# Optimization experiments

Hardware: AMD Instinct MI355X
Metric: run time of the kernel (lower is better)

Reference implementation:

```python
import jax, jax.numpy as jnp
import numpy as np

D = 2048
N = 4096
HEAD = 2
DH = D // HEAD


def setup_inputs() -> dict:
    key = jax.random.key(0)
    ks = jax.random.split(key, 7)
    s = 0.02  # realistic init scale for weights
    x = jax.random.normal(ks[0], (1, N, D), jnp.float32)
    Wq1 = jax.random.normal(ks[1], (DH, DH), jnp.float32) * s
    Wq2 = jax.random.normal(ks[2], (DH, DH), jnp.float32) * s
    Wk1 = jax.random.normal(ks[3], (DH, DH), jnp.float32) * s
    Wk2 = jax.random.normal(ks[4], (DH, DH), jnp.float32) * s
    Wv1 = jax.random.normal(ks[5], (DH, DH), jnp.float32) * s
    Wv2 = jax.random.normal(ks[6], (DH, DH), jnp.float32) * s
    return {"x": x, "Wq1": Wq1, "Wq2": Wq2, "Wk1": Wk1, "Wk2": Wk2,
            "Wv1": Wv1, "Wv2": Wv2}


def _head(xh, Wq, Wk, Wv):
    # xh: [1, N, Dh]; Linear applies in @ W^T (no bias)
    q = (xh @ Wq.T)[0]                      # [N, Dh]
    k = (xh @ Wk.T)[0]                      # [N, Dh] (k reshaped to 2D in torch)
    v = (xh @ Wv.T)[0]                      # [N, Dh]
    # QK_T linear with weight dynamically set to k (detached in torch):
    Sc = q @ jax.lax.stop_gradient(k).T     # [N, N]
    # Sc_V linear on v^T with weight set to Sc (detached in torch):
    Sc = jax.lax.stop_gradient(Sc)
    return v.T @ Sc.T                       # [Dh, N]  == (Sc @ v)^T


def reference(x, Wq1, Wq2, Wk1, Wk2, Wv1, Wv2):
    Dh = Wq1.shape[0]
    x1, x2 = x[..., :Dh], x[..., Dh:]       # torch.chunk(x, 2, dim=2)
    o1 = _head(x1, Wq1, Wk1, Wv1)           # [Dh, N]
    o2 = _head(x2, Wq2, Wk2, Wv2)           # [Dh, N]
    out = jnp.concatenate([o1, o2], axis=0).T  # transpose(-2,-1).squeeze -> [N, D]
    return out
```

## Files before the change

### kernel.cpp

```cpp
#include <hip/hip_runtime.h>
#include <hip/hip_bf16.h>


using bf16 = __hip_bfloat16;
typedef __attribute__((ext_vector_type(8))) __bf16 bf16x8;
typedef __attribute__((ext_vector_type(8))) unsigned short u16x8;
typedef __attribute__((ext_vector_type(4))) float f32x4;

#define M1 (1024 * 1024)

struct GB {
    const bf16* A[8];
    const bf16* B[8];
    void*       C[8];
    int lda[8];
    int ldb[8];
};

__device__ __forceinline__ void gload_lds16(const void* g, void* l) {
    __builtin_amdgcn_global_load_lds(
        (const __attribute__((address_space(1))) void*)g,
        (__attribute__((address_space(3))) void*)l, 16, 0, 0);
}

template<int N>
__device__ __forceinline__ void waitv() {
    if constexpr (N == 4)      asm volatile("s_waitcnt vmcnt(4)" ::: "memory");
    else if constexpr (N == 3) asm volatile("s_waitcnt vmcnt(3)" ::: "memory");
    else                       asm volatile("s_waitcnt vmcnt(0)" ::: "memory");
}

template<int BM_, int BN_, typename OUT_T>
__device__ __forceinline__ void gemm_core(
    const bf16* __restrict__ A, int lda,
    const bf16* __restrict__ B, int ldb,
    OUT_T* __restrict__ C, int ldc,
    int m0, int n0, int Ksub,
    unsigned short* smem, int tid)
{
    auto As = (unsigned short(*)[BM_ * 32])smem;
    auto Bs = (unsigned short(*)[BN_ * 32])(smem + 2 * BM_ * 32);

    constexpr int MI = BM_ / 32;
    constexpr int NI = BN_ / 32;
    constexpr int NLOADS = (BM_ + BN_) / 64;

    const int lane = tid & 63;
    const int wave = tid >> 6;
    const int wm   = wave >> 1;
    const int wn   = wave & 1;
    const int fr = lane & 15;
    const int kg = lane >> 4;
    const int srow = tid >> 2;
    const int scol = (tid & 3) * 8;

    auto stage = [&](int buf, int kt) {
        #pragma unroll
        for (int r = 0; r < BM_ / 64; ++r)
            gload_lds16(A + (size_t)(m0 + r * 64 + srow) * lda + (kt + scol),
                        &As[buf][(r * 64 + srow) * 32 + scol]);
        #pragma unroll
        for (int r = 0; r < BN_ / 64; ++r)
            gload_lds16(B + (size_t)(n0 + r * 64 + srow) * ldb + (kt + scol),
                        &Bs[buf][(r * 64 + srow) * 32 + scol]);
    };

    f32x4 acc[MI][NI];
    #pragma unroll
    for (int i = 0; i < MI; ++i)
        #pragma unroll
        for (int j = 0; j < NI; ++j)
            acc[i][j] = {0.f, 0.f, 0.f, 0.f};

    const int niter = Ksub >> 5;
    int cur = 0;
    stage(0, 0);

    for (int it = 0; it < niter; ++it) {
        if (it + 1 < niter) {
            stage(cur ^ 1, (it + 1) << 5);
            waitv<NLOADS>();
        } else {
            waitv<0>();
        }
        __builtin_amdgcn_s_barrier();
        __builtin_amdgcn_sched_barrier(0);

        bf16x8 afrag[MI], bfrag[NI];
        #pragma unroll
        for (int mi = 0; mi < MI; ++mi)
            afrag[mi] = *(const bf16x8*)&As[cur][(wm * (BM_ / 2) + mi * 16 + fr) * 32 + kg * 8];
        #pragma unroll
        for (int ni = 0; ni < NI; ++ni)
            bfrag[ni] = *(const bf16x8*)&Bs[cur][(wn * (BN_ / 2) + ni * 16 + fr) * 32 + kg * 8];

        #pragma unroll
        for (int mi = 0; mi < MI; ++mi)
            #pragma unroll
            for (int ni = 0; ni < NI; ++ni)
                acc[mi][ni] = __builtin_amdgcn_mfma_f32_16x16x32_bf16(
                    afrag[mi], bfrag[ni], acc[mi][ni], 0, 0, 0);

        __builtin_amdgcn_sched_barrier(0);
        __builtin_amdgcn_s_barrier();
        __builtin_amdgcn_sched_barrier(0);
        cur ^= 1;
    }

    if constexpr (sizeof(OUT_T) == 2) {
        #pragma unroll
        for (int mi = 0; mi < MI; ++mi)
            #pragma unroll
            for (int ni = 0; ni < NI; ++ni) {
                const int c = wn * (BN_ / 2) + ni * 16 + fr;
                #pragma unroll
                for (int j = 0; j < 4; ++j) {
                    const int r = wm * (BM_ / 2) + mi * 16 + kg * 4 + j;
                    bf16 h = __float2bfloat16(acc[mi][ni][j]);
                    smem[r * BN_ + c] = *(unsigned short*)&h;
                }
            }
        __syncthreads();
        constexpr int V = (BM_ * BN_) / 2048;
        #pragma unroll
        for (int v = 0; v < V; ++v) {
            const int off = v * 2048 + tid * 8;
            const int r = off / BN_;
            const int c = off % BN_;
            *(u16x8*)((unsigned short*)C + (size_t)(m0 + r) * ldc + n0 + c) =
                *(const u16x8*)&smem[off];
        }
    } else {
        float* fs = (float*)smem;
        #pragma unroll
        for (int mi = 0; mi < MI; ++mi)
            #pragma unroll
            for (int ni = 0; ni < NI; ++ni) {
                const int c = wn * (BN_ / 2) + ni * 16 + fr;
                #pragma unroll
                for (int j = 0; j < 4; ++j) {
                    const int r = wm * (BM_ / 2) + mi * 16 + kg * 4 + j;
                    fs[r * BN_ + c] = acc[mi][ni][j];
                }
            }
        __syncthreads();
        constexpr int V = (BM_ * BN_) / 1024;
        #pragma unroll
        for (int v = 0; v < V; ++v) {
            const int off = v * 1024 + tid * 4;
            const int r = off / BN_;
            const int c = off % BN_;
            *(float4*)((float*)C + (size_t)(m0 + r) * ldc + n0 + c) =
                *(const float4*)&fs[off];
        }
    }
}

template<int BM_, int BN_, typename OUT_T>
__global__ __launch_bounds__(256, 4)
void gemm_bt_pa(GB g, int Ksub, int ldc)
{
    constexpr int STAGE_SH = 2 * (BM_ + BN_) * 32;
    constexpr int EPI_SH   = BM_ * BN_ * (int)sizeof(OUT_T) / 2;
    constexpr int SMEM_SH  = STAGE_SH > EPI_SH ? STAGE_SH : EPI_SH;
    __shared__ __align__(16) unsigned short smem[SMEM_SH];

    const int gx = gridDim.x, gy = gridDim.y;
    const int nwg = gx * gy * gridDim.z;
    const int orig = blockIdx.x + gx * (blockIdx.y + gy * blockIdx.z);
    const int cpx = nwg >> 3;
    const int wg = (orig & 7) * cpx + (orig >> 3);
    const int bx = wg % gx;
    const int by = (wg / gx) % gy;
    const int bz = wg / (gx * gy);

    gemm_core<BM_, BN_, OUT_T>(g.A[bz], g.lda[bz], g.B[bz], g.ldb[bz],
                               (OUT_T*)g.C[bz], ldc,
                               by * BM_, bx * BN_, Ksub,
                               smem, threadIdx.x);
}

struct B1Args {
    const bf16* xt;
    const bf16* wdst;
    bf16* Gp;
    bf16* Mp;
};

__global__ __launch_bounds__(256, 4)
void b1_kernel(B1Args a)
{
    __shared__ __align__(16) unsigned short smem[16384];

    const int nwg = 832;
    const int orig = blockIdx.x + 52 * blockIdx.z;
    const int cpx = nwg >> 3;
    const int wg = (orig & 7) * cpx + (orig >> 3);
    const int bx = wg % 52;
    const int bz = wg / 52;

    if (bx < 36) {
        const int h = bz >> 3, s = bz & 7;
        int ti = 0, rem = bx;
        while (rem >= 8 - ti) { rem -= 8 - ti; ++ti; }
        const int tj = ti + rem;
        const bf16* A = a.xt + (size_t)(h * 1024 + ti * 128) * 4096 + s * 512;
        const bf16* B = a.xt + (size_t)(h * 1024 + tj * 128) * 4096 + s * 512;
        bf16* C = a.Gp + ((size_t)bz * 36 + bx) * 16384;
        gemm_core<128, 128, bf16>(A, 4096, B, 4096, C, 128, 0, 0, 512,
                                  smem, threadIdx.x);
    } else {
        const int combo = bz & 3;
        const int h = combo >> 1, s = combo & 1;
        const int tile = (bz >> 2) * 16 + (bx - 36);
        const int m0 = (tile >> 3) * 128;
        const int n0 = (tile & 7) * 128;
        const bf16* A = a.wdst + (size_t)h * M1 + s * 512;
        const bf16* B = a.wdst + (size_t)(2 + h) * M1 + s * 512;
        bf16* C = a.Mp + (size_t)combo * M1;
        gemm_core<128, 128, bf16>(A, 1024, B, 1024, C, 1024, m0, n0, 512,
                                  smem, threadIdx.x);
    }
}


__device__ __forceinline__ ushort4 cvt4(float4 v) {
    ushort4 o; bf16 h;
    h = __float2bfloat16(v.x); o.x = *(unsigned short*)&h;
    h = __float2bfloat16(v.y); o.y = *(unsigned short*)&h;
    h = __float2bfloat16(v.z); o.z = *(unsigned short*)&h;
    h = __float2bfloat16(v.w); o.w = *(unsigned short*)&h;
    return o;
}

struct PrepArgs {
    const float* x;
    const float* w[4];
    const float* wv[2];
    bf16* xb;
    bf16* xt;
    bf16* wdst;
};

__device__ void xpose64(const float* __restrict__ src, int ldsrc,
                        int r0, int c0,
                        bf16* __restrict__ dstS, int ldS,
                        bf16* __restrict__ dstT, int ldT,
                        float (*tile)[65], int t)
{
    const int tr  = t >> 4;
    const int tc4 = (t & 15) * 4;
    #pragma unroll
    for (int ph = 0; ph < 4; ++ph) {
        const int row = ph * 16 + tr;
        float4 v = *(const float4*)(src + (size_t)(r0 + row) * ldsrc + c0 + tc4);
        tile[row][tc4 + 0] = v.x;
        tile[row][tc4 + 1] = v.y;
        tile[row][tc4 + 2] = v.z;
        tile[row][tc4 + 3] = v.w;
        if (dstS)
            *(ushort4*)((unsigned short*)dstS + (size_t)(r0 + row) * ldS + c0 + tc4) = cvt4(v);
    }
    __syncthreads();
    #pragma unroll
    for (int ph = 0; ph < 4; ++ph) {
        const int crow = ph * 16 + tr;
        float4 v = {tile[tc4 + 0][crow], tile[tc4 + 1][crow],
                    tile[tc4 + 2][crow], tile[tc4 + 3][crow]};
        *(ushort4*)((unsigned short*)dstT + (size_t)(c0 + crow) * ldT + r0 + tc4) = cvt4(v);
    }
}

__global__ void prep(PrepArgs p)
{
    __shared__ float tile[64][65];
    const int b = blockIdx.x;
    const int t = threadIdx.x;

    if (b < 2048) {
        const int n0 = (b & 63) * 64;
        const int c0 = (b >> 6) * 64;
        xpose64(p.x, 2048, n0, c0, p.xb, 2048, p.xt, 4096, tile, t);
    } else if (b < 3072) {
        const int i = b - 2048;
        const int mat = i >> 8;
        const int tl  = i & 255;
        const int r0 = (tl & 15) * 64;
        const int c0 = (tl >> 4) * 64;
        xpose64(p.w[mat], 1024, r0, c0, nullptr, 0,
                p.wdst + (size_t)mat * M1, 1024, tile, t);
    } else {
        const int i = b - 3072;
        const int mat = i >> 9;
        const int blk = i & 511;
        const size_t off = (size_t)blk * 2048 + t * 8;
        float4 v0 = *(const float4*)(p.wv[mat] + off);
        float4 v1 = *(const float4*)(p.wv[mat] + off + 4);
        unsigned short* d = (unsigned short*)p.wdst + (size_t)(4 + mat) * M1 + off;
        *(ushort4*)d       = cvt4(v0);
        *(ushort4*)(d + 4) = cvt4(v1);
    }
}


__device__ __forceinline__ void reduce_slices(const unsigned short* src,
                                              unsigned short* dst,
                                              int h, int r, int nslice)
{
    float acc[8] = {0, 0, 0, 0, 0, 0, 0, 0};
    for (int s = 0; s < nslice; ++s) {
        u16x8 v = *(const u16x8*)(src + ((size_t)(h * nslice + s) << 20) + r);
        #pragma unroll
        for (int j = 0; j < 8; ++j)
            acc[j] += __uint_as_float(((unsigned)v[j]) << 16);
    }
    u16x8 o;
    #pragma unroll
    for (int j = 0; j < 8; ++j) {
        bf16 hh = __float2bfloat16(acc[j]);
        o[j] = *(unsigned short*)&hh;
    }
    *(u16x8*)(dst + ((size_t)h << 20) + r) = o;
}

__global__ void reduce_GM(const unsigned short* Gp, const unsigned short* Mp,
                          unsigned short* Gd, unsigned short* Md)
{
    const int b = blockIdx.x, t = threadIdx.x;
    if (b < 576) {
        const int h    = b / 288;
        const int rem  = b - h * 288;
        const int tile = rem >> 3;
        const int blk  = rem & 7;
        int ti = 0, trem = tile;
        while (trem >= 8 - ti) { trem -= 8 - ti; ++ti; }
        const int tj = ti + trem;

        const int e  = blk * 2048 + t * 8;
        const int r  = e >> 7;
        const int c0 = e & 127;

        float acc[8] = {0, 0, 0, 0, 0, 0, 0, 0};
        for (int s = 0; s < 8; ++s) {
            u16x8 v = *(const u16x8*)(Gp + ((size_t)(h * 8 + s) * 36 + tile) * 16384 + e);
            #pragma unroll
            for (int j = 0; j < 8; ++j)
                acc[j] += __uint_as_float(((unsigned)v[j]) << 16);
        }
        u16x8 o;
        #pragma unroll
        for (int j = 0; j < 8; ++j) {
            bf16 hh = __float2bfloat16(acc[j]);
            o[j] = *(unsigned short*)&hh;
        }
        unsigned short* G = Gd + (size_t)h * M1;
        *(u16x8*)(G + (size_t)(ti * 128 + r) * 1024 + tj * 128 + c0) = o;
        if (ti != tj) {
            #pragma unroll
            for (int j = 0; j < 8; ++j)
                G[(size_t)(tj * 128 + c0 + j) * 1024 + ti * 128 + r] = o[j];
        }
    } else {
        const int e = ((b - 576) * 256 + t) * 8;
        reduce_slices(Mp, Md, e >> 20, e & (M1 - 1), 2);
    }
}

__global__ void reduce_4(const unsigned short* Sp, unsigned short* Dd)
{
    const int e = (blockIdx.x * 256 + threadIdx.x) * 8;
    reduce_slices(Sp, Dd, e >> 20, e & (M1 - 1), 4);
}


extern "C" void kernel_launch(void* const* d_in, const int* in_sizes, int n_in,
                              void* d_out, int out_size, void* d_ws, size_t ws_size,
                              hipStream_t stream)
{
    bf16* xb   = (bf16*)d_ws;
    bf16* xt   = xb + 8 * M1;
    bf16* wdst = xt + 8 * M1;
    bf16* Mp   = wdst + 6 * M1;
    bf16* Mb   = Mp + 4 * M1;
    bf16* Gb   = Mb + 2 * M1;
    bf16* Ytb  = Gb + 2 * M1;
    bf16* Utb  = Ytb + 2 * M1;

    bf16* scr = (bf16*)d_out;

    PrepArgs pa;
    pa.x = (const float*)d_in[0];
    pa.w[0] = (const float*)d_in[1];  pa.w[1] = (const float*)d_in[2];
    pa.w[2] = (const float*)d_in[3];  pa.w[3] = (const float*)d_in[4];
    pa.wv[0] = (const float*)d_in[5]; pa.wv[1] = (const float*)d_in[6];
    pa.xb = xb; pa.xt = xt; pa.wdst = wdst;
    prep<<<4096, 256, 0, stream>>>(pa);

    B1Args b1;
    b1.xt = xt; b1.wdst = wdst; b1.Gp = scr; b1.Mp = Mp;
    b1_kernel<<<dim3(52, 1, 16), 256, 0, stream>>>(b1);

    reduce_GM<<<1600, 256, 0, stream>>>((const unsigned short*)scr,
                                        (const unsigned short*)Mp,
                                        (unsigned short*)Gb, (unsigned short*)Mb);

    GB g;

    for (int z = 0; z < 8; ++z) {
        const int h = z >> 2, s = z & 3;
        g.A[z] = Mb + (size_t)h * M1 + s * 256;  g.lda[z] = 1024;
        g.B[z] = Gb + (size_t)h * M1 + s * 256;  g.ldb[z] = 1024;
        g.C[z] = (bf16*)scr + (size_t)z * M1;
    }
    gemm_bt_pa<128, 128, bf16><<<dim3(8, 8, 8), 256, 0, stream>>>(g, 256, 1024);

    reduce_4<<<1024, 256, 0, stream>>>((const unsigned short*)scr, (unsigned short*)Ytb);

    for (int z = 0; z < 8; ++z) {
        const int h = z >> 2, s = z & 3;
        g.A[z] = wdst + (size_t)(4 + h) * M1 + s * 256;  g.lda[z] = 1024;
        g.B[z] = Ytb + (size_t)h * M1 + s * 256;         g.ldb[z] = 1024;
        g.C[z] = (bf16*)scr + (size_t)z * M1;
    }
    gemm_bt_pa<128, 128, bf16><<<dim3(8, 8, 8), 256, 0, stream>>>(g, 256, 1024);

    reduce_4<<<1024, 256, 0, stream>>>((const unsigned short*)scr, (unsigned short*)Utb);

    for (int z = 0; z < 2; ++z) {
        g.A[z] = xb + (size_t)z * 1024;   g.lda[z] = 2048;
        g.B[z] = Utb + (size_t)z * M1;    g.ldb[z] = 1024;
        g.C[z] = (float*)d_out + (size_t)z * 1024;
    }
    gemm_bt_pa<128, 64, float><<<dim3(16, 32, 2), 256, 0, stream>>>(g, 1024, 2048);
}
```

Baseline: 119.9 us.

## Use BK=64 swizzled single-buffer GEMM core and drop split-K for M product

The GEMM core moves from a double-buffered BK=32 pipeline to a single-buffered BK=64 tile. LDS columns are XOR-swizzled to avoid bank conflicts, and each iteration runs two MFMA k-steps. The weight-product GEMM no longer splits K in two, so it writes Mb directly, and the separate M reduction and its partial buffer go away. Work is flattened to a 1D grid of 704 blocks. The cost is losing overlap between global loads and compute, since each iteration now waits for vmcnt(0) before computing.

```diff
diff --git a/kernel.cpp b/kernel.cpp
--- a/kernel.cpp
+++ b/kernel.cpp
@@ -23,11 +23,8 @@
         (__attribute__((address_space(3))) void*)l, 16, 0, 0);
 }
 
-template<int N>
-__device__ __forceinline__ void waitv() {
-    if constexpr (N == 4)      asm volatile("s_waitcnt vmcnt(4)" ::: "memory");
-    else if constexpr (N == 3) asm volatile("s_waitcnt vmcnt(3)" ::: "memory");
-    else                       asm volatile("s_waitcnt vmcnt(0)" ::: "memory");
+__device__ __forceinline__ void waitv0() {
+    asm volatile("s_waitcnt vmcnt(0)" ::: "memory");
 }
 
 template<int BM_, int BN_, typename OUT_T>
@@ -38,12 +35,12 @@
     int m0, int n0, int Ksub,
     unsigned short* smem, int tid)
 {
-    auto As = (unsigned short(*)[BM_ * 32])smem;
-    auto Bs = (unsigned short(*)[BN_ * 32])(smem + 2 * BM_ * 32);
+    constexpr int BK = 64;
+    unsigned short* As = smem;
+    unsigned short* Bs = smem + BM_ * BK;
 
     constexpr int MI = BM_ / 32;
     constexpr int NI = BN_ / 32;
-    constexpr int NLOADS = (BM_ + BN_) / 64;
 
     const int lane = tid & 63;
     const int wave = tid >> 6;
@@ -51,19 +48,10 @@
     const int wn   = wave & 1;
     const int fr = lane & 15;
     const int kg = lane >> 4;
-    const int srow = tid >> 2;
-    const int scol = (tid & 3) * 8;
-
-    auto stage = [&](int buf, int kt) {
-        #pragma unroll
-        for (int r = 0; r < BM_ / 64; ++r)
-            gload_lds16(A + (size_t)(m0 + r * 64 + srow) * lda + (kt + scol),
-                        &As[buf][(r * 64 + srow) * 32 + scol]);
-        #pragma unroll
-        for (int r = 0; r < BN_ / 64; ++r)
-            gload_lds16(B + (size_t)(n0 + r * 64 + srow) * ldb + (kt + scol),
-                        &Bs[buf][(r * 64 + srow) * 32 + scol]);
-    };
+
+    const int srow  = tid >> 3;
+    const int scol  = (tid & 7) * 8;
+    const int scolg = scol ^ ((srow & 7) << 3);
 
     f32x4 acc[MI][NI];
     #pragma unroll
@@ -72,39 +60,47 @@
         for (int j = 0; j < NI; ++j)
             acc[i][j] = {0.f, 0.f, 0.f, 0.f};
 
-    const int niter = Ksub >> 5;
-    int cur = 0;
-    stage(0, 0);
-
+    const int niter = Ksub >> 6;
     for (int it = 0; it < niter; ++it) {
-        if (it + 1 < niter) {
-            stage(cur ^ 1, (it + 1) << 5);
-            waitv<NLOADS>();
-        } else {
-            waitv<0>();
-        }
+        const int kt = it << 6;
+        #pragma unroll
+        for (int r = 0; r < BM_ / 32; ++r)
+            gload_lds16(A + (size_t)(m0 + r * 32 + srow) * lda + (kt + scolg),
+                        &As[(r * 32 + srow) * BK + scol]);
+        #pragma unroll
+        for (int r = 0; r < BN_ / 32; ++r)
+            gload_lds16(B + (size_t)(n0 + r * 32 + srow) * ldb + (kt + scolg),
+                        &Bs[(r * 32 + srow) * BK + scol]);
+        waitv0();
         __builtin_amdgcn_s_barrier();
         __builtin_amdgcn_sched_barrier(0);
 
-        bf16x8 afrag[MI], bfrag[NI];
-        #pragma unroll
-        for (int mi = 0; mi < MI; ++mi)
-            afrag[mi] = *(const bf16x8*)&As[cur][(wm * (BM_ / 2) + mi * 16 + fr) * 32 + kg * 8];
-        #pragma unroll
-        for (int ni = 0; ni < NI; ++ni)
-            bfrag[ni] = *(const bf16x8*)&Bs[cur][(wn * (BN_ / 2) + ni * 16 + fr) * 32 + kg * 8];
-
-        #pragma unroll
-        for (int mi = 0; mi < MI; ++mi)
+        #pragma unroll
+        for (int kk = 0; kk < 2; ++kk) {
+            bf16x8 af[MI], bfg[NI];
             #pragma unroll
-            for (int ni = 0; ni < NI; ++ni)
-                acc[mi][ni] = __builtin_amdgcn_mfma_f32_16x16x32_bf16(
-                    afrag[mi], bfrag[ni], acc[mi][ni], 0, 0, 0);
+            for (int mi = 0; mi < MI; ++mi) {
+                const int row = wm * (BM_ / 2) + mi * 16 + fr;
+                const int c = (kk * 32 + kg * 8) ^ ((row & 7) << 3);
+                af[mi] = *(const bf16x8*)&As[row * BK + c];
+            }
+            #pragma unroll
+            for (int ni = 0; ni < NI; ++ni) {
+                const int row = wn * (BN_ / 2) + ni * 16 + fr;
+                const int c = (kk * 32 + kg * 8) ^ ((row & 7) << 3);
+                bfg[ni] = *(const bf16x8*)&Bs[row * BK + c];
+            }
+            #pragma unroll
+            for (int mi = 0; mi < MI; ++mi)
+                #pragma unroll
+                for (int ni = 0; ni < NI; ++ni)
+                    acc[mi][ni] = __builtin_amdgcn_mfma_f32_16x16x32_bf16(
+                        af[mi], bfg[ni], acc[mi][ni], 0, 0, 0);
+        }
 
         __builtin_amdgcn_sched_barrier(0);
         __builtin_amdgcn_s_barrier();
         __builtin_amdgcn_sched_barrier(0);
-        cur ^= 1;
     }
 
     if constexpr (sizeof(OUT_T) == 2) {
@@ -160,7 +156,7 @@
 __global__ __launch_bounds__(256, 4)
 void gemm_bt_pa(GB g, int Ksub, int ldc)
 {
-    constexpr int STAGE_SH = 2 * (BM_ + BN_) * 32;
+    constexpr int STAGE_SH = (BM_ + BN_) * 64;
     constexpr int EPI_SH   = BM_ * BN_ * (int)sizeof(OUT_T) / 2;
     constexpr int SMEM_SH  = STAGE_SH > EPI_SH ? STAGE_SH : EPI_SH;
     __shared__ __align__(16) unsigned short smem[SMEM_SH];
@@ -184,7 +180,7 @@
     const bf16* xt;
     const bf16* wdst;
     bf16* Gp;
-    bf16* Mp;
+    bf16* Mb;
 };
 
 __global__ __launch_bounds__(256, 4)
@@ -192,33 +188,33 @@
 {
     __shared__ __align__(16) unsigned short smem[16384];
 
-    const int nwg = 832;
-    const int orig = blockIdx.x + 52 * blockIdx.z;
+    const int nwg = 704;
+    const int orig = blockIdx.x;
     const int cpx = nwg >> 3;
     const int wg = (orig & 7) * cpx + (orig >> 3);
-    const int bx = wg % 52;
-    const int bz = wg / 52;
-
-    if (bx < 36) {
-        const int h = bz >> 3, s = bz & 7;
-        int ti = 0, rem = bx;
+
+    if (wg < 576) {
+        const int z = wg / 36;
+        const int tile = wg - z * 36;
+        const int h = z >> 3, s = z & 7;
+        int ti = 0, rem = tile;
         while (rem >= 8 - ti) { rem -= 8 - ti; ++ti; }
         const int tj = ti + rem;
         const bf16* A = a.xt + (size_t)(h * 1024 + ti * 128) * 4096 + s * 512;
         const bf16* B = a.xt + (size_t)(h * 1024 + tj * 128) * 4096 + s * 512;
-        bf16* C = a.Gp + ((size_t)bz * 36 + bx) * 16384;
+        bf16* C = a.Gp + ((size_t)z * 36 + tile) * 16384;
         gemm_core<128, 128, bf16>(A, 4096, B, 4096, C, 128, 0, 0, 512,
                                   smem, threadIdx.x);
     } else {
-        const int combo = bz & 3;
-        const int h = combo >> 1, s = combo & 1;
-        const int tile = (bz >> 2) * 16 + (bx - 36);
+        const int idx = wg - 576;
+        const int h = idx >> 6;
+        const int tile = idx & 63;
         const int m0 = (tile >> 3) * 128;
         const int n0 = (tile & 7) * 128;
-        const bf16* A = a.wdst + (size_t)h * M1 + s * 512;
-        const bf16* B = a.wdst + (size_t)(2 + h) * M1 + s * 512;
-        bf16* C = a.Mp + (size_t)combo * M1;
-        gemm_core<128, 128, bf16>(A, 1024, B, 1024, C, 1024, m0, n0, 512,
+        const bf16* A = a.wdst + (size_t)h * M1;
+        const bf16* B = a.wdst + (size_t)(2 + h) * M1;
+        bf16* C = a.Mb + (size_t)h * M1;
+        gemm_core<128, 128, bf16>(A, 1024, B, 1024, C, 1024, m0, n0, 1024,
                                   smem, threadIdx.x);
     }
 }
@@ -323,46 +319,40 @@
     *(u16x8*)(dst + ((size_t)h << 20) + r) = o;
 }
 
-__global__ void reduce_GM(const unsigned short* Gp, const unsigned short* Mp,
-                          unsigned short* Gd, unsigned short* Md)
+__global__ void reduce_G(const unsigned short* Gp, unsigned short* Gd)
 {
     const int b = blockIdx.x, t = threadIdx.x;
-    if (b < 576) {
-        const int h    = b / 288;
-        const int rem  = b - h * 288;
-        const int tile = rem >> 3;
-        const int blk  = rem & 7;
-        int ti = 0, trem = tile;
-        while (trem >= 8 - ti) { trem -= 8 - ti; ++ti; }
-        const int tj = ti + trem;
-
-        const int e  = blk * 2048 + t * 8;
-        const int r  = e >> 7;
-        const int c0 = e & 127;
-
-        float acc[8] = {0, 0, 0, 0, 0, 0, 0, 0};
-        for (int s = 0; s < 8; ++s) {
-            u16x8 v = *(const u16x8*)(Gp + ((size_t)(h * 8 + s) * 36 + tile) * 16384 + e);
-            #pragma unroll
-            for (int j = 0; j < 8; ++j)
-                acc[j] += __uint_as_float(((unsigned)v[j]) << 16);
-        }
-        u16x8 o;
-        #pragma unroll
-        for (int j = 0; j < 8; ++j) {
-            bf16 hh = __float2bfloat16(acc[j]);
-            o[j] = *(unsigned short*)&hh;
-        }
-        unsigned short* G = Gd + (size_t)h * M1;
-        *(u16x8*)(G + (size_t)(ti * 128 + r) * 1024 + tj * 128 + c0) = o;
-        if (ti != tj) {
-            #pragma unroll
-            for (int j = 0; j < 8; ++j)
-                G[(size_t)(tj * 128 + c0 + j) * 1024 + ti * 128 + r] = o[j];
-        }
-    } else {
-        const int e = ((b - 576) * 256 + t) * 8;
-        reduce_slices(Mp, Md, e >> 20, e & (M1 - 1), 2);
+    const int h    = b / 288;
+    const int rem  = b - h * 288;
+    const int tile = rem >> 3;
+    const int blk  = rem & 7;
+    int ti = 0, trem = tile;
+    while (trem >= 8 - ti) { trem -= 8 - ti; ++ti; }
+    const int tj = ti + trem;
+
+    const int e  = blk * 2048 + t * 8;
+    const int r  = e >> 7;
+    const int c0 = e & 127;
+
+    float acc[8] = {0, 0, 0, 0, 0, 0, 0, 0};
+    for (int s = 0; s < 8; ++s) {
+        u16x8 v = *(const u16x8*)(Gp + ((size_t)(h * 8 + s) * 36 + tile) * 16384 + e);
+        #pragma unroll
+        for (int j = 0; j < 8; ++j)
+            acc[j] += __uint_as_float(((unsigned)v[j]) << 16);
+    }
+    u16x8 o;
+    #pragma unroll
+    for (int j = 0; j < 8; ++j) {
+        bf16 hh = __float2bfloat16(acc[j]);
+        o[j] = *(unsigned short*)&hh;
+    }
+    unsigned short* G = Gd + (size_t)h * M1;
+    *(u16x8*)(G + (size_t)(ti * 128 + r) * 1024 + tj * 128 + c0) = o;
+    if (ti != tj) {
+        #pragma unroll
+        for (int j = 0; j < 8; ++j)
+            G[(size_t)(tj * 128 + c0 + j) * 1024 + ti * 128 + r] = o[j];
     }
 }
 
@@ -380,8 +370,7 @@
     bf16* xb   = (bf16*)d_ws;
     bf16* xt   = xb + 8 * M1;
     bf16* wdst = xt + 8 * M1;
-    bf16* Mp   = wdst + 6 * M1;
-    bf16* Mb   = Mp + 4 * M1;
+    bf16* Mb   = wdst + 6 * M1;
     bf16* Gb   = Mb + 2 * M1;
     bf16* Ytb  = Gb + 2 * M1;
     bf16* Utb  = Ytb + 2 * M1;
@@ -397,12 +386,11 @@
     prep<<<4096, 256, 0, stream>>>(pa);
 
     B1Args b1;
-    b1.xt = xt; b1.wdst = wdst; b1.Gp = scr; b1.Mp = Mp;
-    b1_kernel<<<dim3(52, 1, 16), 256, 0, stream>>>(b1);
-
-    reduce_GM<<<1600, 256, 0, stream>>>((const unsigned short*)scr,
-                                        (const unsigned short*)Mp,
-                                        (unsigned short*)Gb, (unsigned short*)Mb);
+    b1.xt = xt; b1.wdst = wdst; b1.Gp = scr; b1.Mb = Mb;
+    b1_kernel<<<704, 256, 0, stream>>>(b1);
+
+    reduce_G<<<576, 256, 0, stream>>>((const unsigned short*)scr,
+                                      (unsigned short*)Gb);
 
     GB g;
 
```

Measured after the change: 115.3 us. 3.8% less time.
